# Kernel optimization log

Measured on AMD Instinct MI355X. Metric: run time of the kernel, lower is better.

## Reference

```python
import jax, jax.numpy as jnp
import numpy as np

# dims: M=MC samples, B=graphs, K=latent, H=decoder hidden, N=max nodes, P=permutations
M, B, K, H, N, F_DIM, P = 4, 256, 64, 1024, 50, 3, 64
E = N * (N - 1) // 2  # reduced adjacency = strictly lower triangle
COEFF_A = 1.0
BETA = 1.0
TRIL_I, TRIL_J = np.tril_indices(N, -1)


def setup_inputs() -> dict:
    key = jax.random.key(0)
    ks = jax.random.split(key, 12)
    mean = 0.5 * jax.random.normal(ks[0], (B, K), dtype=jnp.float32)
    logvar = 0.1 * jax.random.normal(ks[1], (B, K), dtype=jnp.float32)
    eps = jax.random.normal(ks[2], (M, B, K), dtype=jnp.float32)
    W1 = jax.random.normal(ks[3], (K, H), dtype=jnp.float32) / np.sqrt(K)
    b1 = jnp.zeros((H,), jnp.float32)
    WA = jax.random.normal(ks[4], (H, E), dtype=jnp.float32) / np.sqrt(H)
    bA = jnp.zeros((E,), jnp.float32)
    WF = jax.random.normal(ks[5], (H, N * F_DIM), dtype=jnp.float32) / np.sqrt(H)
    bF = jnp.zeros((N * F_DIM,), jnp.float32)
    # symmetric binary adjacency with zero diagonal
    U = jax.random.bernoulli(ks[6], 0.15, (B, N, N)).astype(jnp.float32)
    Au = jnp.triu(U, 1)
    A_in = Au + jnp.swapaxes(Au, -1, -2)
    # two bernoulli attributes + one one-hot-categorical attribute (over nodes)
    fb = jax.random.bernoulli(ks[7], 0.3, (B, N, 2)).astype(jnp.float32)
    idx = jax.random.randint(ks[8], (B,), 0, N)
    oh = jax.nn.one_hot(idx, N, dtype=jnp.float32)  # (B, N)
    Fx = jnp.concatenate([fb, oh[..., None]], axis=-1)  # (B, N, 3)
    coeff_Fx = jnp.ones((F_DIM,), jnp.float32)
    permutations = jax.vmap(lambda k: jax.random.permutation(k, N))(
        jax.random.split(ks[9], P)).astype(jnp.int32)  # (P, N)
    return dict(mean=mean, logvar=logvar, eps=eps, W1=W1, b1=b1, WA=WA, bA=bA,
                WF=WF, bF=bF, A_in=A_in, Fx=Fx, coeff_Fx=coeff_Fx,
                permutations=permutations)


def _bernoulli_logprob(x, logits):
    # sum of elementwise Bernoulli log-prob over last axis
    return jnp.sum(x * jax.nn.log_sigmoid(logits)
                   + (1.0 - x) * jax.nn.log_sigmoid(-logits), axis=-1)


def reference(mean, logvar, eps, W1, b1, WA, bA, WF, bF, A_in, Fx, coeff_Fx,
              permutations):
    # pathwise (reparametrised) latent samples: (M, B, K)
    Z = mean + jnp.exp(0.5 * logvar) * eps
    # MLP decoder
    h = jax.nn.relu(Z @ W1 + b1)                       # (M, B, H)
    logits_A = h @ WA + bA                              # (M, B, E)
    logits_Fx = (h @ WF + bF).reshape(M, B, N, F_DIM)   # (M, B, N, F)
    # permutation-matched adjacency: A_perm[b,p,i,j] = A_in[b, perm[p,i], perm[p,j]]
    A_perm = A_in[:, permutations[:, :, None], permutations[:, None, :]]  # (B,P,N,N)
    A_red = A_perm[..., TRIL_I, TRIL_J].reshape(B * P, E)                 # (B*P, E)
    lA = jnp.repeat(logits_A, P, axis=1)                                  # (M, B*P, E)
    nce_A = _bernoulli_logprob(A_red, lA).mean(axis=0)                    # (B*P,)
    nce_A = nce_A.reshape(B, P).max(axis=1)                               # (B,)
    # attribute log-probs: two bernoulli (sum over nodes), one categorical over nodes
    lp_bern = jnp.sum(
        Fx[..., :2] * jax.nn.log_sigmoid(logits_Fx[..., :2])
        + (1.0 - Fx[..., :2]) * jax.nn.log_sigmoid(-logits_Fx[..., :2]),
        axis=-2)                                                          # (M, B, 2)
    lp_cat = jnp.sum(Fx[..., 2] * jax.nn.log_softmax(logits_Fx[..., 2], axis=-1),
                     axis=-1)                                             # (M, B)
    nce_Fx = jnp.concatenate([lp_bern.mean(0), lp_cat.mean(0)[:, None]], axis=-1)  # (B, F)
    # KL(q(z|x) || N(0, I))
    kld = 0.5 * jnp.sum(jnp.exp(logvar) + mean ** 2 - 1.0 - logvar, axis=-1)  # (B,)
    return COEFF_A * nce_A + nce_Fx @ coeff_Fx - BETA * kld
```

## Files before the change

### kernel.cpp

```cpp
#include <hip/hip_runtime.h>
#include <math.h>

#define MM 4
#define BB 256
#define KK 64
#define HH 1024
#define NN 50
#define EE 1225
#define PP 64
#define CTOT 1375
#define NPAD 1408

typedef short short8 __attribute__((ext_vector_type(8)));
typedef float floatx4 __attribute__((ext_vector_type(4)));
typedef unsigned short ushort;

__device__ __forceinline__ ushort f2bf(float f) {
    union { float f; unsigned u; } v; v.f = f;
    unsigned r = v.u + 0x7fffu + ((v.u >> 16) & 1u);
    return (ushort)(r >> 16);
}

__device__ __forceinline__ float logsigm(float l) {
    return -(fmaxf(l, 0.0f) + log1pf(expf(-fabsf(l))));
}

__device__ __forceinline__ float wsum64(float v) {
    #pragma unroll
    for (int m = 1; m < 64; m <<= 1) v += __shfl_xor(v, m);
    return v;
}
__device__ __forceinline__ float wmax64(float v) {
    #pragma unroll
    for (int m = 1; m < 64; m <<= 1) v = fmaxf(v, __shfl_xor(v, m));
    return v;
}

__global__ __launch_bounds__(256) void kA(const float* __restrict__ mean,
                                          const float* __restrict__ logvar,
                                          const float* __restrict__ eps,
                                          const float* __restrict__ W1,
                                          const float* __restrict__ b1,
                                          const float* __restrict__ WA,
                                          const float* __restrict__ WF,
                                          ushort* __restrict__ hB,
                                          ushort* __restrict__ Wt,
                                          float* __restrict__ Sneg) {
    const int t = threadIdx.x;
    __shared__ float smem[64 * 65];

    if (blockIdx.x < 256) {
        const int b = blockIdx.x;
        float4* z4 = (float4*)smem;
        if (t < 64) {
            float mv = mean[b * 64 + t];
            float lv = logvar[b * 64 + t];
            float sd = expf(0.5f * lv);
            float4 z;
            z.x = mv + sd * eps[(0 * BB + b) * 64 + t];
            z.y = mv + sd * eps[(1 * BB + b) * 64 + t];
            z.z = mv + sd * eps[(2 * BB + b) * 64 + t];
            z.w = mv + sd * eps[(3 * BB + b) * 64 + t];
            z4[t] = z;
        }
        if (t < 4) Sneg[b * 4 + t] = 0.0f;
        __syncthreads();
        const int j0 = t * 4;
        float acc[4][4] = {};
        #pragma unroll 8
        for (int k = 0; k < 64; k++) {
            float4 w = *(const float4*)&W1[k * HH + j0];
            float4 z = z4[k];
            acc[0][0] += z.x * w.x; acc[0][1] += z.x * w.y; acc[0][2] += z.x * w.z; acc[0][3] += z.x * w.w;
            acc[1][0] += z.y * w.x; acc[1][1] += z.y * w.y; acc[1][2] += z.y * w.z; acc[1][3] += z.y * w.w;
            acc[2][0] += z.z * w.x; acc[2][1] += z.z * w.y; acc[2][2] += z.z * w.z; acc[2][3] += z.z * w.w;
            acc[3][0] += z.w * w.x; acc[3][1] += z.w * w.y; acc[3][2] += z.w * w.z; acc[3][3] += z.w * w.w;
        }
        float4 bb = *(const float4*)&b1[j0];
        #pragma unroll
        for (int m = 0; m < 4; m++) {
            unsigned u0 = ((unsigned)f2bf(fmaxf(acc[m][0] + bb.x, 0.f))) |
                          ((unsigned)f2bf(fmaxf(acc[m][1] + bb.y, 0.f)) << 16);
            unsigned u1 = ((unsigned)f2bf(fmaxf(acc[m][2] + bb.z, 0.f))) |
                          ((unsigned)f2bf(fmaxf(acc[m][3] + bb.w, 0.f)) << 16);
            uint2 u; u.x = u0; u.y = u1;
            *(uint2*)&hB[(b * 4 + m) * HH + j0] = u;
        }
    } else {
        const int id = blockIdx.x - 256;
        const int kt = id & 15, nt = id >> 4;
        float* T = smem;
        const int k0 = kt * 64, n0 = nt * 64;
        #pragma unroll
        for (int i = 0; i < 16; i++) {
            int x = i * 256 + t;
            int kk = x >> 6, nn = x & 63;
            int gn = n0 + nn, gk = k0 + kk;
            float v = 0.f;
            if (gn < EE)        v = WA[gk * EE + gn];
            else if (gn < CTOT) v = WF[gk * 150 + (gn - EE)];
            T[kk * 65 + nn] = v;
        }
        __syncthreads();
        #pragma unroll
        for (int i = 0; i < 16; i++) {
            int x = i * 256 + t;
            int nn = x >> 6, kk = x & 63;
            Wt[(n0 + nn) * 1024 + k0 + kk] = f2bf(T[kk * 65 + nn]);
        }
    }
}

__global__ __launch_bounds__(256) void k2(const ushort* __restrict__ hB,
                                          const ushort* __restrict__ Wt,
                                          const float* __restrict__ bA,
                                          const float* __restrict__ bF,
                                          float* __restrict__ Lbar,
                                          float* __restrict__ Sneg,
                                          float* __restrict__ lgF) {
    const int ct = blockIdx.x;
    const int rt = blockIdx.y;
    const int t = threadIdx.x;
    const int w = t >> 6, lane = t & 63;
    const int wm = w >> 1, wn = w & 1;
    const int quad = lane >> 4, l16 = lane & 15;
    __shared__ short As[64][72];
    __shared__ short Bs[128][72];
    floatx4 acc[2][4] = {};
    const int row0 = rt * 64, col0 = ct * 128;

    const int rA0 = t >> 3,              koA = (t & 7) * 8;
    const int rA1 = (256 + t) >> 3;
    const int rB0 = t >> 3;
    const ushort* pA0 = hB + (row0 + rA0) * 1024 + koA;
    const ushort* pA1 = hB + (row0 + rA1) * 1024 + koA;
    const ushort* pB  = Wt + (col0 + rB0) * 1024 + koA;

    short8 ra[2], rb[4];
    ra[0] = *(const short8*)(pA0);
    ra[1] = *(const short8*)(pA1);
    #pragma unroll
    for (int i = 0; i < 4; i++) rb[i] = *(const short8*)(pB + i * 32 * 1024);

    for (int ch = 0; ch < 16; ch++) {
        __syncthreads();
        *(short8*)&As[rA0][koA] = ra[0];
        *(short8*)&As[rA1][koA] = ra[1];
        #pragma unroll
        for (int i = 0; i < 4; i++) *(short8*)&Bs[i * 32 + rB0][koA] = rb[i];
        __syncthreads();
        if (ch < 15) {
            const int off = (ch + 1) * 64;
            ra[0] = *(const short8*)(pA0 + off);
            ra[1] = *(const short8*)(pA1 + off);
            #pragma unroll
            for (int i = 0; i < 4; i++) rb[i] = *(const short8*)(pB + i * 32 * 1024 + off);
        }
        #pragma unroll
        for (int kk = 0; kk < 2; kk++) {
            int ko = kk * 32 + quad * 8;
            short8 a0 = *(const short8*)&As[wm * 32 + l16][ko];
            short8 a1 = *(const short8*)&As[wm * 32 + 16 + l16][ko];
            short8 b0 = *(const short8*)&Bs[wn * 64 + l16][ko];
            short8 b1 = *(const short8*)&Bs[wn * 64 + 16 + l16][ko];
            short8 b2 = *(const short8*)&Bs[wn * 64 + 32 + l16][ko];
            short8 b3 = *(const short8*)&Bs[wn * 64 + 48 + l16][ko];
            acc[0][0] = __builtin_amdgcn_mfma_f32_16x16x32_bf16(a0, b0, acc[0][0], 0, 0, 0);
            acc[0][1] = __builtin_amdgcn_mfma_f32_16x16x32_bf16(a0, b1, acc[0][1], 0, 0, 0);
            acc[0][2] = __builtin_amdgcn_mfma_f32_16x16x32_bf16(a0, b2, acc[0][2], 0, 0, 0);
            acc[0][3] = __builtin_amdgcn_mfma_f32_16x16x32_bf16(a0, b3, acc[0][3], 0, 0, 0);
            acc[1][0] = __builtin_amdgcn_mfma_f32_16x16x32_bf16(a1, b0, acc[1][0], 0, 0, 0);
            acc[1][1] = __builtin_amdgcn_mfma_f32_16x16x32_bf16(a1, b1, acc[1][1], 0, 0, 0);
            acc[1][2] = __builtin_amdgcn_mfma_f32_16x16x32_bf16(a1, b2, acc[1][2], 0, 0, 0);
            acc[1][3] = __builtin_amdgcn_mfma_f32_16x16x32_bf16(a1, b3, acc[1][3], 0, 0, 0);
        }
    }

    #pragma unroll
    for (int mi = 0; mi < 2; mi++) {
        const int grow = row0 + wm * 32 + mi * 16 + quad * 4;
        const int b = grow >> 2;
        float sn0 = 0.f, sn1 = 0.f, sn2 = 0.f, sn3 = 0.f;
        #pragma unroll
        for (int ni = 0; ni < 4; ni++) {
            int gc = col0 + wn * 64 + ni * 16 + l16;
            floatx4 a = acc[mi][ni];
            if (gc < EE) {
                float bias = bA[gc];
                float l0 = a[0] + bias, l1 = a[1] + bias, l2 = a[2] + bias, l3 = a[3] + bias;
                Lbar[b * EE + gc] = 0.25f * (l0 + l1 + l2 + l3);
                sn0 += logsigm(l0); sn1 += logsigm(l1); sn2 += logsigm(l2); sn3 += logsigm(l3);
            } else if (gc < CTOT) {
                int c2 = gc - EE;
                float bias = bF[c2];
                lgF[(b * 4 + 0) * 150 + c2] = a[0] + bias;
                lgF[(b * 4 + 1) * 150 + c2] = a[1] + bias;
                lgF[(b * 4 + 2) * 150 + c2] = a[2] + bias;
                lgF[(b * 4 + 3) * 150 + c2] = a[3] + bias;
            }
        }
        #pragma unroll
        for (int msk = 1; msk < 16; msk <<= 1) {
            sn0 += __shfl_xor(sn0, msk);
            sn1 += __shfl_xor(sn1, msk);
            sn2 += __shfl_xor(sn2, msk);
            sn3 += __shfl_xor(sn3, msk);
        }
        if (l16 == 0) {
            atomicAdd(&Sneg[b * 4 + 0], sn0);
            atomicAdd(&Sneg[b * 4 + 1], sn1);
            atomicAdd(&Sneg[b * 4 + 2], sn2);
            atomicAdd(&Sneg[b * 4 + 3], sn3);
        }
    }
}

__global__ __launch_bounds__(256) void k4(const float* __restrict__ mean,
                                          const float* __restrict__ logvar,
                                          const float* __restrict__ A,
                                          const float* __restrict__ Fx,
                                          const float* __restrict__ coeff,
                                          const int* __restrict__ perms,
                                          const float* __restrict__ Lbar,
                                          const float* __restrict__ Sneg,
                                          const float* __restrict__ lgF,
                                          float* __restrict__ out) {
    const int b = blockIdx.x;
    const int t = threadIdx.x;
    const int w = t >> 6, lane = t & 63;
    __shared__ int   ip[PP * NN];
    __shared__ float Lb[EE];
    __shared__ int   edges[1280];
    __shared__ float lgfs[600];
    __shared__ int   nE;
    __shared__ float mred[4], wmaxs[4], klds;

    if (t == 0) nE = 0;
    for (int x = t; x < PP * NN; x += 256) {
        int p = x / NN, i = x - p * NN;
        ip[p * NN + perms[x]] = i;
    }
    for (int x = t; x < EE; x += 256) Lb[x] = Lbar[b * EE + x];
    for (int x = t; x < 600; x += 256) lgfs[x] = lgF[b * 600 + x];
    __syncthreads();

    for (int e = t; e < EE; e += 256) {
        int i = (int)((1.0f + sqrtf(8.0f * (float)e + 1.0f)) * 0.5f);
        while (i * (i - 1) / 2 > e) i--;
        while (i * (i + 1) / 2 <= e) i++;
        int j = e - i * (i - 1) / 2;
        float a = A[b * 2500 + i * NN + j];
        if (a != 0.0f) { int id = atomicAdd(&nE, 1); edges[id] = (i << 8) | j; }
    }

    {
        float l0 = 0.f, l1 = 0.f, l2 = -INFINITY, x0 = 0.f, x1 = 0.f, x2 = 0.f;
        bool v = lane < NN;
        if (v) {
            l0 = lgfs[w * 150 + lane * 3 + 0];
            l1 = lgfs[w * 150 + lane * 3 + 1];
            l2 = lgfs[w * 150 + lane * 3 + 2];
            x0 = Fx[b * 150 + lane * 3 + 0];
            x1 = Fx[b * 150 + lane * 3 + 1];
            x2 = Fx[b * 150 + lane * 3 + 2];
        }
        float mx = wmax64(l2);
        float es = v ? expf(l2 - mx) : 0.f;
        es = wsum64(es);
        float lse = mx + logf(es);
        float val = 0.f;
        if (v) {
            val = coeff[0] * (logsigm(l0) + x0 * l0)
                + coeff[1] * (logsigm(l1) + x1 * l1)
                + coeff[2] * (x2 * (l2 - lse));
        }
        val = wsum64(val);
        if (lane == 0) mred[w] = val;
    }
    if (w == 0) {
        float lv = logvar[b * 64 + lane];
        float mn = mean[b * 64 + lane];
        float term = 0.5f * (expf(lv) + mn * mn - 1.0f - lv);
        term = wsum64(term);
        if (lane == 0) klds = term;
    }
    __syncthreads();

    const int ne = nE;
    float lmax = -INFINITY;
    for (int p = w; p < PP; p += 4) {
        const int* ipp = &ip[p * NN];
        float acc = 0.f;
        for (int x = lane; x < ne; x += 64) {
            int ed = edges[x];
            int iu = ipp[ed >> 8], iv = ipp[ed & 255];
            int ii = max(iu, iv), jj = min(iu, iv);
            acc += Lb[ii * (ii - 1) / 2 + jj];
        }
        acc = wsum64(acc);
        lmax = fmaxf(lmax, acc);
    }
    if (lane == 0) wmaxs[w] = lmax;
    __syncthreads();
    if (t == 0) {
        float dmax = fmaxf(fmaxf(wmaxs[0], wmaxs[1]), fmaxf(wmaxs[2], wmaxs[3]));
        float sbar = 0.25f * (Sneg[b * 4 + 0] + Sneg[b * 4 + 1] + Sneg[b * 4 + 2] + Sneg[b * 4 + 3]);
        float fxv  = 0.25f * (mred[0] + mred[1] + mred[2] + mred[3]);
        out[b] = (sbar + dmax) + fxv - klds;
    }
}

extern "C" void kernel_launch(void* const* d_in, const int* in_sizes, int n_in,
                              void* d_out, int out_size, void* d_ws, size_t ws_size,
                              hipStream_t stream) {
    const float* mean   = (const float*)d_in[0];
    const float* logvar = (const float*)d_in[1];
    const float* eps    = (const float*)d_in[2];
    const float* W1     = (const float*)d_in[3];
    const float* b1     = (const float*)d_in[4];
    const float* WA     = (const float*)d_in[5];
    const float* bA     = (const float*)d_in[6];
    const float* WF     = (const float*)d_in[7];
    const float* bF     = (const float*)d_in[8];
    const float* A      = (const float*)d_in[9];
    const float* Fx     = (const float*)d_in[10];
    const float* coeff  = (const float*)d_in[11];
    const int*   perms  = (const int*)d_in[12];
    float* out = (float*)d_out;

    ushort* Wt  = (ushort*)d_ws;
    ushort* hB  = Wt + NPAD * 1024;
    float*  Lbar = (float*)(hB + 1024 * 1024);
    float*  Sneg = Lbar + BB * EE;
    float*  lgF  = Sneg + 1024;

    kA<<<dim3(608), dim3(256), 0, stream>>>(mean, logvar, eps, W1, b1, WA, WF, hB, Wt, Sneg);
    k2<<<dim3(11, 16), dim3(256), 0, stream>>>(hB, Wt, bA, bF, Lbar, Sneg, lgF);
    k4<<<dim3(BB), dim3(256), 0, stream>>>(mean, logvar, A, Fx, coeff, perms, Lbar, Sneg, lgF, out);
}
```

Baseline: 138.3 us.

## Fuse three kernels into one cooperative persistent kernel with grid syncs

Replaces the three launches (hidden layer plus weight transpose, MFMA GEMM, per-graph reduction) with one cooperative kernel of 256 blocks that uses grid-wide syncs between the phases. This removes two launch gaps and the pipeline drains between kernels. The GEMM phase now double-buffers its LDS tiles with one barrier per chunk, and edge extraction scans the full matrix instead of inverting the triangular index. The costs are fewer blocks doing the weight transpose (352 tiles over 256 blocks instead of a dedicated grid), only 176 of 256 blocks busy during the GEMM, and the overhead of the grid syncs. If the cooperative launch fails, the original three kernels run instead.

```diff
diff --git a/kernel.cpp b/kernel.cpp
--- a/kernel.cpp
+++ b/kernel.cpp
@@ -1,5 +1,8 @@
 #include <hip/hip_runtime.h>
+#include <hip/hip_cooperative_groups.h>
 #include <math.h>
+
+namespace cg = cooperative_groups;
 
 #define MM 4
 #define BB 256
@@ -34,6 +37,283 @@
     #pragma unroll
     for (int m = 1; m < 64; m <<= 1) v = fmaxf(v, __shfl_xor(v, m));
     return v;
+}
+
+struct SMg { short As[2][64][72]; short Bs[2][128][72]; };
+struct SMf {
+    int   ip[PP * NN];
+    float Lb[EE];
+    int   edges[1280];
+    float lgfs[600];
+    int   nE;
+    float mred[4], wmaxs[4], klds;
+};
+union SMem {
+    SMg    g;
+    float  T[64 * 65];
+    float4 z4[64];
+    SMf    f;
+};
+
+__global__ __launch_bounds__(256, 1) void mega(
+        const float* __restrict__ mean, const float* __restrict__ logvar,
+        const float* __restrict__ eps,  const float* __restrict__ W1,
+        const float* __restrict__ b1,   const float* __restrict__ WA,
+        const float* __restrict__ WF,   const float* __restrict__ bA,
+        const float* __restrict__ bF,   const float* __restrict__ A,
+        const float* __restrict__ Fx,   const float* __restrict__ coeff,
+        const int*   __restrict__ perms,
+        ushort* __restrict__ hB, ushort* __restrict__ Wt,
+        float* __restrict__ Lbar, float* __restrict__ Sneg,
+        float* __restrict__ lgF,  float* __restrict__ out) {
+    __shared__ SMem sm;
+    const int bid = blockIdx.x;
+    const int t = threadIdx.x;
+
+    {
+        const int b = bid;
+        if (t < 64) {
+            float mv = mean[b * 64 + t];
+            float lv = logvar[b * 64 + t];
+            float sd = expf(0.5f * lv);
+            float4 z;
+            z.x = mv + sd * eps[(0 * BB + b) * 64 + t];
+            z.y = mv + sd * eps[(1 * BB + b) * 64 + t];
+            z.z = mv + sd * eps[(2 * BB + b) * 64 + t];
+            z.w = mv + sd * eps[(3 * BB + b) * 64 + t];
+            sm.z4[t] = z;
+        }
+        if (t < 4) Sneg[b * 4 + t] = 0.0f;
+        __syncthreads();
+        const int j0 = t * 4;
+        float acc[4][4] = {};
+        #pragma unroll 8
+        for (int k = 0; k < 64; k++) {
+            float4 w = *(const float4*)&W1[k * HH + j0];
+            float4 z = sm.z4[k];
+            acc[0][0] += z.x * w.x; acc[0][1] += z.x * w.y; acc[0][2] += z.x * w.z; acc[0][3] += z.x * w.w;
+            acc[1][0] += z.y * w.x; acc[1][1] += z.y * w.y; acc[1][2] += z.y * w.z; acc[1][3] += z.y * w.w;
+            acc[2][0] += z.z * w.x; acc[2][1] += z.z * w.y; acc[2][2] += z.z * w.z; acc[2][3] += z.z * w.w;
+            acc[3][0] += z.w * w.x; acc[3][1] += z.w * w.y; acc[3][2] += z.w * w.z; acc[3][3] += z.w * w.w;
+        }
+        float4 bb = *(const float4*)&b1[j0];
+        #pragma unroll
+        for (int m = 0; m < 4; m++) {
+            unsigned u0 = ((unsigned)f2bf(fmaxf(acc[m][0] + bb.x, 0.f))) |
+                          ((unsigned)f2bf(fmaxf(acc[m][1] + bb.y, 0.f)) << 16);
+            unsigned u1 = ((unsigned)f2bf(fmaxf(acc[m][2] + bb.z, 0.f))) |
+                          ((unsigned)f2bf(fmaxf(acc[m][3] + bb.w, 0.f)) << 16);
+            uint2 u; u.x = u0; u.y = u1;
+            *(uint2*)&hB[(b * 4 + m) * HH + j0] = u;
+        }
+        __syncthreads();
+
+        for (int id = bid; id < 352; id += 256) {
+            const int kt = id & 15, nt = id >> 4;
+            const int k0 = kt * 64, n0 = nt * 64;
+            #pragma unroll
+            for (int i = 0; i < 16; i++) {
+                int x = i * 256 + t;
+                int kk = x >> 6, nn = x & 63;
+                int gn = n0 + nn, gk = k0 + kk;
+                float v = 0.f;
+                if (gn < EE)        v = WA[gk * EE + gn];
+                else if (gn < CTOT) v = WF[gk * 150 + (gn - EE)];
+                sm.T[kk * 65 + nn] = v;
+            }
+            __syncthreads();
+            #pragma unroll
+            for (int i = 0; i < 16; i++) {
+                int x = i * 256 + t;
+                int nn = x >> 6, kk = x & 63;
+                Wt[(n0 + nn) * 1024 + k0 + kk] = f2bf(sm.T[kk * 65 + nn]);
+            }
+            __syncthreads();
+        }
+    }
+
+    cg::this_grid().sync();
+
+    if (bid < 176) {
+        const int ct = bid % 11;
+        const int rt = bid / 11;
+        const int w = t >> 6, lane = t & 63;
+        const int wm = w >> 1, wn = w & 1;
+        const int quad = lane >> 4, l16 = lane & 15;
+        floatx4 acc[2][4] = {};
+        const int row0 = rt * 64, col0 = ct * 128;
+
+        const int rA0 = t >> 3, koA = (t & 7) * 8;
+        const int rA1 = rA0 + 32;
+        const int rB0 = t >> 3;
+        const ushort* pA0 = hB + (row0 + rA0) * 1024 + koA;
+        const ushort* pA1 = hB + (row0 + rA1) * 1024 + koA;
+        const ushort* pB  = Wt + (col0 + rB0) * 1024 + koA;
+
+        short8 ra0, ra1, rb[4];
+        ra0 = *(const short8*)(pA0);
+        ra1 = *(const short8*)(pA1);
+        #pragma unroll
+        for (int i = 0; i < 4; i++) rb[i] = *(const short8*)(pB + i * 32 * 1024);
+        *(short8*)&sm.g.As[0][rA0][koA] = ra0;
+        *(short8*)&sm.g.As[0][rA1][koA] = ra1;
+        #pragma unroll
+        for (int i = 0; i < 4; i++) *(short8*)&sm.g.Bs[0][i * 32 + rB0][koA] = rb[i];
+
+        for (int ch = 0; ch < 16; ch++) {
+            if (ch < 15) {
+                const int off = (ch + 1) * 64;
+                ra0 = *(const short8*)(pA0 + off);
+                ra1 = *(const short8*)(pA1 + off);
+                #pragma unroll
+                for (int i = 0; i < 4; i++) rb[i] = *(const short8*)(pB + i * 32 * 1024 + off);
+            }
+            __syncthreads();
+            const int cur = ch & 1;
+            #pragma unroll
+            for (int kk = 0; kk < 2; kk++) {
+                int ko = kk * 32 + quad * 8;
+                short8 a0 = *(const short8*)&sm.g.As[cur][wm * 32 + l16][ko];
+                short8 a1 = *(const short8*)&sm.g.As[cur][wm * 32 + 16 + l16][ko];
+                short8 b0 = *(const short8*)&sm.g.Bs[cur][wn * 64 + l16][ko];
+                short8 b1 = *(const short8*)&sm.g.Bs[cur][wn * 64 + 16 + l16][ko];
+                short8 b2 = *(const short8*)&sm.g.Bs[cur][wn * 64 + 32 + l16][ko];
+                short8 b3 = *(const short8*)&sm.g.Bs[cur][wn * 64 + 48 + l16][ko];
+                acc[0][0] = __builtin_amdgcn_mfma_f32_16x16x32_bf16(a0, b0, acc[0][0], 0, 0, 0);
+                acc[0][1] = __builtin_amdgcn_mfma_f32_16x16x32_bf16(a0, b1, acc[0][1], 0, 0, 0);
+                acc[0][2] = __builtin_amdgcn_mfma_f32_16x16x32_bf16(a0, b2, acc[0][2], 0, 0, 0);
+                acc[0][3] = __builtin_amdgcn_mfma_f32_16x16x32_bf16(a0, b3, acc[0][3], 0, 0, 0);
+                acc[1][0] = __builtin_amdgcn_mfma_f32_16x16x32_bf16(a1, b0, acc[1][0], 0, 0, 0);
+                acc[1][1] = __builtin_amdgcn_mfma_f32_16x16x32_bf16(a1, b1, acc[1][1], 0, 0, 0);
+                acc[1][2] = __builtin_amdgcn_mfma_f32_16x16x32_bf16(a1, b2, acc[1][2], 0, 0, 0);
+                acc[1][3] = __builtin_amdgcn_mfma_f32_16x16x32_bf16(a1, b3, acc[1][3], 0, 0, 0);
+            }
+            if (ch < 15) {
+                const int nxt = cur ^ 1;
+                *(short8*)&sm.g.As[nxt][rA0][koA] = ra0;
+                *(short8*)&sm.g.As[nxt][rA1][koA] = ra1;
+                #pragma unroll
+                for (int i = 0; i < 4; i++) *(short8*)&sm.g.Bs[nxt][i * 32 + rB0][koA] = rb[i];
+            }
+        }
+
+        #pragma unroll
+        for (int mi = 0; mi < 2; mi++) {
+            const int grow = row0 + wm * 32 + mi * 16 + quad * 4;
+            const int b = grow >> 2;
+            float sn0 = 0.f, sn1 = 0.f, sn2 = 0.f, sn3 = 0.f;
+            #pragma unroll
+            for (int ni = 0; ni < 4; ni++) {
+                int gc = col0 + wn * 64 + ni * 16 + l16;
+                floatx4 a = acc[mi][ni];
+                if (gc < EE) {
+                    float bias = bA[gc];
+                    float l0 = a[0] + bias, l1 = a[1] + bias, l2 = a[2] + bias, l3 = a[3] + bias;
+                    Lbar[b * EE + gc] = 0.25f * (l0 + l1 + l2 + l3);
+                    sn0 += logsigm(l0); sn1 += logsigm(l1); sn2 += logsigm(l2); sn3 += logsigm(l3);
+                } else if (gc < CTOT) {
+                    int c2 = gc - EE;
+                    float bias = bF[c2];
+                    lgF[(b * 4 + 0) * 150 + c2] = a[0] + bias;
+                    lgF[(b * 4 + 1) * 150 + c2] = a[1] + bias;
+                    lgF[(b * 4 + 2) * 150 + c2] = a[2] + bias;
+                    lgF[(b * 4 + 3) * 150 + c2] = a[3] + bias;
+                }
+            }
+            #pragma unroll
+            for (int msk = 1; msk < 16; msk <<= 1) {
+                sn0 += __shfl_xor(sn0, msk);
+                sn1 += __shfl_xor(sn1, msk);
+                sn2 += __shfl_xor(sn2, msk);
+                sn3 += __shfl_xor(sn3, msk);
+            }
+            if (l16 == 0) {
+                atomicAdd(&Sneg[b * 4 + 0], sn0);
+                atomicAdd(&Sneg[b * 4 + 1], sn1);
+                atomicAdd(&Sneg[b * 4 + 2], sn2);
+                atomicAdd(&Sneg[b * 4 + 3], sn3);
+            }
+        }
+    }
+
+    cg::this_grid().sync();
+
+    {
+        const int b = bid;
+        const int w = t >> 6, lane = t & 63;
+        if (t == 0) sm.f.nE = 0;
+        for (int x = t; x < PP * NN; x += 256) {
+            int p = x / NN, i = x - p * NN;
+            sm.f.ip[p * NN + perms[x]] = i;
+        }
+        for (int x = t; x < EE; x += 256) sm.f.Lb[x] = Lbar[b * EE + x];
+        for (int x = t; x < 600; x += 256) sm.f.lgfs[x] = lgF[b * 600 + x];
+        __syncthreads();
+
+        for (int x = t; x < 2500; x += 256) {
+            int i = x / NN, j = x - i * NN;
+            if (j < i) {
+                float a = A[b * 2500 + x];
+                if (a != 0.0f) { int id = atomicAdd(&sm.f.nE, 1); sm.f.edges[id] = (i << 8) | j; }
+            }
+        }
+
+        {
+            float l0 = 0.f, l1 = 0.f, l2 = -INFINITY, x0 = 0.f, x1 = 0.f, x2 = 0.f;
+            bool v = lane < NN;
+            if (v) {
+                l0 = sm.f.lgfs[w * 150 + lane * 3 + 0];
+                l1 = sm.f.lgfs[w * 150 + lane * 3 + 1];
+                l2 = sm.f.lgfs[w * 150 + lane * 3 + 2];
+                x0 = Fx[b * 150 + lane * 3 + 0];
+                x1 = Fx[b * 150 + lane * 3 + 1];
+                x2 = Fx[b * 150 + lane * 3 + 2];
+            }
+            float mx = wmax64(l2);
+            float es = v ? expf(l2 - mx) : 0.f;
+            es = wsum64(es);
+            float lse = mx + logf(es);
+            float val = 0.f;
+            if (v) {
+                val = coeff[0] * (logsigm(l0) + x0 * l0)
+                    + coeff[1] * (logsigm(l1) + x1 * l1)
+                    + coeff[2] * (x2 * (l2 - lse));
+            }
+            val = wsum64(val);
+            if (lane == 0) sm.f.mred[w] = val;
+        }
+        if (w == 0) {
+            float lv = logvar[b * 64 + lane];
+            float mn = mean[b * 64 + lane];
+            float term = 0.5f * (expf(lv) + mn * mn - 1.0f - lv);
+            term = wsum64(term);
+            if (lane == 0) sm.f.klds = term;
+        }
+        __syncthreads();
+
+        const int ne = sm.f.nE;
+        float lmax = -INFINITY;
+        for (int p = w; p < PP; p += 4) {
+            const int* ipp = &sm.f.ip[p * NN];
+            float acc = 0.f;
+            for (int x = lane; x < ne; x += 64) {
+                int ed = sm.f.edges[x];
+                int iu = ipp[ed >> 8], iv = ipp[ed & 255];
+                int ii = max(iu, iv), jj = min(iu, iv);
+                acc += sm.f.Lb[ii * (ii - 1) / 2 + jj];
+            }
+            acc = wsum64(acc);
+            lmax = fmaxf(lmax, acc);
+        }
+        if (lane == 0) sm.f.wmaxs[w] = lmax;
+        __syncthreads();
+        if (t == 0) {
+            float dmax = fmaxf(fmaxf(sm.f.wmaxs[0], sm.f.wmaxs[1]), fmaxf(sm.f.wmaxs[2], sm.f.wmaxs[3]));
+            float sbar = 0.25f * (Sneg[b * 4 + 0] + Sneg[b * 4 + 1] + Sneg[b * 4 + 2] + Sneg[b * 4 + 3]);
+            float fxv  = 0.25f * (sm.f.mred[0] + sm.f.mred[1] + sm.f.mred[2] + sm.f.mred[3]);
+            out[b] = (sbar + dmax) + fxv - sm.f.klds;
+        }
+    }
 }
 
 __global__ __launch_bounds__(256) void kA(const float* __restrict__ mean,
@@ -48,7 +328,6 @@
                                           float* __restrict__ Sneg) {
     const int t = threadIdx.x;
     __shared__ float smem[64 * 65];
-
     if (blockIdx.x < 256) {
         const int b = blockIdx.x;
         float4* z4 = (float4*)smem;
@@ -128,20 +407,17 @@
     __shared__ short Bs[128][72];
     floatx4 acc[2][4] = {};
     const int row0 = rt * 64, col0 = ct * 128;
-
-    const int rA0 = t >> 3,              koA = (t & 7) * 8;
+    const int rA0 = t >> 3, koA = (t & 7) * 8;
     const int rA1 = (256 + t) >> 3;
     const int rB0 = t >> 3;
     const ushort* pA0 = hB + (row0 + rA0) * 1024 + koA;
     const ushort* pA1 = hB + (row0 + rA1) * 1024 + koA;
     const ushort* pB  = Wt + (col0 + rB0) * 1024 + koA;
-
     short8 ra[2], rb[4];
     ra[0] = *(const short8*)(pA0);
     ra[1] = *(const short8*)(pA1);
     #pragma unroll
     for (int i = 0; i < 4; i++) rb[i] = *(const short8*)(pB + i * 32 * 1024);
-
     for (int ch = 0; ch < 16; ch++) {
         __syncthreads();
         *(short8*)&As[rA0][koA] = ra[0];
@@ -175,7 +451,6 @@
             acc[1][3] = __builtin_amdgcn_mfma_f32_16x16x32_bf16(a1, b3, acc[1][3], 0, 0, 0);
         }
     }
-
     #pragma unroll
     for (int mi = 0; mi < 2; mi++) {
         const int grow = row0 + wm * 32 + mi * 16 + quad * 4;
@@ -228,38 +503,29 @@
     const int b = blockIdx.x;
     const int t = threadIdx.x;
     const int w = t >> 6, lane = t & 63;
-    __shared__ int   ip[PP * NN];
-    __shared__ float Lb[EE];
-    __shared__ int   edges[1280];
-    __shared__ float lgfs[600];
-    __shared__ int   nE;
-    __shared__ float mred[4], wmaxs[4], klds;
-
-    if (t == 0) nE = 0;
+    __shared__ SMf f;
+    if (t == 0) f.nE = 0;
     for (int x = t; x < PP * NN; x += 256) {
         int p = x / NN, i = x - p * NN;
-        ip[p * NN + perms[x]] = i;
-    }
-    for (int x = t; x < EE; x += 256) Lb[x] = Lbar[b * EE + x];
-    for (int x = t; x < 600; x += 256) lgfs[x] = lgF[b * 600 + x];
+        f.ip[p * NN + perms[x]] = i;
+    }
+    for (int x = t; x < EE; x += 256) f.Lb[x] = Lbar[b * EE + x];
+    for (int x = t; x < 600; x += 256) f.lgfs[x] = lgF[b * 600 + x];
     __syncthreads();
-
-    for (int e = t; e < EE; e += 256) {
-        int i = (int)((1.0f + sqrtf(8.0f * (float)e + 1.0f)) * 0.5f);
-        while (i * (i - 1) / 2 > e) i--;
-        while (i * (i + 1) / 2 <= e) i++;
-        int j = e - i * (i - 1) / 2;
-        float a = A[b * 2500 + i * NN + j];
-        if (a != 0.0f) { int id = atomicAdd(&nE, 1); edges[id] = (i << 8) | j; }
-    }
-
+    for (int x = t; x < 2500; x += 256) {
+        int i = x / NN, j = x - i * NN;
+        if (j < i) {
+            float a = A[b * 2500 + x];
+            if (a != 0.0f) { int id = atomicAdd(&f.nE, 1); f.edges[id] = (i << 8) | j; }
+        }
+    }
     {
         float l0 = 0.f, l1 = 0.f, l2 = -INFINITY, x0 = 0.f, x1 = 0.f, x2 = 0.f;
         bool v = lane < NN;
         if (v) {
-            l0 = lgfs[w * 150 + lane * 3 + 0];
-            l1 = lgfs[w * 150 + lane * 3 + 1];
-            l2 = lgfs[w * 150 + lane * 3 + 2];
+            l0 = f.lgfs[w * 150 + lane * 3 + 0];
+            l1 = f.lgfs[w * 150 + lane * 3 + 1];
+            l2 = f.lgfs[w * 150 + lane * 3 + 2];
             x0 = Fx[b * 150 + lane * 3 + 0];
             x1 = Fx[b * 150 + lane * 3 + 1];
             x2 = Fx[b * 150 + lane * 3 + 2];
@@ -275,38 +541,37 @@
                 + coeff[2] * (x2 * (l2 - lse));
         }
         val = wsum64(val);
-        if (lane == 0) mred[w] = val;
+        if (lane == 0) f.mred[w] = val;
     }
     if (w == 0) {
         float lv = logvar[b * 64 + lane];
         float mn = mean[b * 64 + lane];
         float term = 0.5f * (expf(lv) + mn * mn - 1.0f - lv);
         term = wsum64(term);
-        if (lane == 0) klds = term;
+        if (lane == 0) f.klds = term;
     }
     __syncthreads();
-
-    const int ne = nE;
+    const int ne = f.nE;
     float lmax = -INFINITY;
     for (int p = w; p < PP; p += 4) {
-        const int* ipp = &ip[p * NN];
+        const int* ipp = &f.ip[p * NN];
         float acc = 0.f;
         for (int x = lane; x < ne; x += 64) {
-            int ed = edges[x];
+            int ed = f.edges[x];
             int iu = ipp[ed >> 8], iv = ipp[ed & 255];
             int ii = max(iu, iv), jj = min(iu, iv);
-            acc += Lb[ii * (ii - 1) / 2 + jj];
+            acc += f.Lb[ii * (ii - 1) / 2 + jj];
         }
         acc = wsum64(acc);
         lmax = fmaxf(lmax, acc);
     }
-    if (lane == 0) wmaxs[w] = lmax;
+    if (lane == 0) f.wmaxs[w] = lmax;
     __syncthreads();
     if (t == 0) {
-        float dmax = fmaxf(fmaxf(wmaxs[0], wmaxs[1]), fmaxf(wmaxs[2], wmaxs[3]));
+        float dmax = fmaxf(fmaxf(f.wmaxs[0], f.wmaxs[1]), fmaxf(f.wmaxs[2], f.wmaxs[3]));
         float sbar = 0.25f * (Sneg[b * 4 + 0] + Sneg[b * 4 + 1] + Sneg[b * 4 + 2] + Sneg[b * 4 + 3]);
-        float fxv  = 0.25f * (mred[0] + mred[1] + mred[2] + mred[3]);
-        out[b] = (sbar + dmax) + fxv - klds;
+        float fxv  = 0.25f * (f.mred[0] + f.mred[1] + f.mred[2] + f.mred[3]);
+        out[b] = (sbar + dmax) + fxv - f.klds;
     }
 }
 
@@ -328,13 +593,20 @@
     const int*   perms  = (const int*)d_in[12];
     float* out = (float*)d_out;
 
-    ushort* Wt  = (ushort*)d_ws;
-    ushort* hB  = Wt + NPAD * 1024;
+    ushort* Wt   = (ushort*)d_ws;
+    ushort* hB   = Wt + NPAD * 1024;
     float*  Lbar = (float*)(hB + 1024 * 1024);
     float*  Sneg = Lbar + BB * EE;
     float*  lgF  = Sneg + 1024;
 
-    kA<<<dim3(608), dim3(256), 0, stream>>>(mean, logvar, eps, W1, b1, WA, WF, hB, Wt, Sneg);
-    k2<<<dim3(11, 16), dim3(256), 0, stream>>>(hB, Wt, bA, bF, Lbar, Sneg, lgF);
-    k4<<<dim3(BB), dim3(256), 0, stream>>>(mean, logvar, A, Fx, coeff, perms, Lbar, Sneg, lgF, out);
-}
+    void* args[] = { (void*)&mean, (void*)&logvar, (void*)&eps, (void*)&W1, (void*)&b1,
+                     (void*)&WA, (void*)&WF, (void*)&bA, (void*)&bF, (void*)&A,
+                     (void*)&Fx, (void*)&coeff, (void*)&perms,
+                     (void*)&hB, (void*)&Wt, (void*)&Lbar, (void*)&Sneg, (void*)&lgF, (void*)&out };
+    hipError_t e = hipLaunchCooperativeKernel((void*)mega, dim3(256), dim3(256), args, 0, stream);
+    if (e != hipSuccess) {
+        kA<<<dim3(608), dim3(256), 0, stream>>>(mean, logvar, eps, W1, b1, WA, WF, hB, Wt, Sneg);
+        k2<<<dim3(11, 16), dim3(256), 0, stream>>>(hB, Wt, bA, bF, Lbar, Sneg, lgF);
+        k4<<<dim3(BB), dim3(256), 0, stream>>>(mean, logvar, A, Fx, coeff, perms, Lbar, Sneg, lgF, out);
+    }
+}
```

Result: slower. 216.4 us (+56.5%).
